# Performance work log

Measured on AMD Instinct MI355X. Metric: run time of the kernel, lower is better.

## Reference

```python
import jax, jax.numpy as jnp
import numpy as np
from jax import lax

FILTER_SIZE = 3
C_IN = 128
C_OUT = 256
PAD = 1
STRIDE = 1


def setup_inputs() -> dict:
    key = jax.random.key(0)
    k1, k2 = jax.random.split(key)
    prev_a = jax.random.normal(k1, (32, 56, 56, C_IN), dtype=jnp.float32)
    # filter_w initialized ~ N(0, 1) as in the original tf.random.normal
    filter_w = jax.random.normal(k2, (FILTER_SIZE, FILTER_SIZE, C_IN, C_OUT), dtype=jnp.float32)
    filter_b = jnp.zeros((1, 1, 1, C_OUT), dtype=jnp.float32)
    return {"prev_a": prev_a, "filter_w": filter_w, "filter_b": filter_b}


def reference(prev_a, filter_w, filter_b):
    # NHWC input, HWIO filter -> NHWC output; same math as the nested-loop conv:
    # z[i,h,w,c] = sum(prev_a_pad[i, h*s:h*s+f, w*s:w*s+f, :] * W[:,:,:,c]) + b[c]
    z = lax.conv_general_dilated(
        prev_a,
        filter_w,
        window_strides=(STRIDE, STRIDE),
        padding=[(PAD, PAD), (PAD, PAD)],
        dimension_numbers=("NHWC", "HWIO", "NHWC"),
    )
    z = z + filter_b  # bias broadcast over (m, H, W)
    return jax.nn.relu(z)
```

## Files before the change

kernel.cpp:

```cpp
#include <hip/hip_runtime.h>
#include <hip/hip_bf16.h>


#define NIMG 32
#define HH 56
#define WW 56
#define PH 58
#define PW 58
#define CIN 128
#define COUT 256
#define KTOT 1152
#define PAD_ELEMS (NIMG * PH * PW * CIN)

#define BM 224
#define BK 64
#define NT (KTOT / BK)
#define NBLK ((NIMG * HH * WW) / BM)

#define AREG_SZ 7168
#define BREG_BASE 28672
#define BREG_SZ 8192

typedef __attribute__((ext_vector_type(8))) short bf16x8;
typedef __attribute__((ext_vector_type(4))) short s16x4;
typedef __attribute__((ext_vector_type(4))) float f32x4;

__device__ __forceinline__ short f2bf(float x) {
    union { __hip_bfloat16 b; short s; } u;
    u.b = __float2bfloat16(x);
    return u.s;
}

typedef const void __attribute__((address_space(1)))* gas1_t;
typedef void __attribute__((address_space(3)))* las3_t;
__device__ __forceinline__ void async16(short* lds_p, const short* g) {
    __builtin_amdgcn_global_load_lds((gas1_t)g, (las3_t)lds_p, 16, 0, 0);
}

__global__ __launch_bounds__(256) void pack_input(const float* __restrict__ in,
                                                  short* __restrict__ pad) {
    const int tid  = blockIdx.x * 256 + threadIdx.x;
    const int flat = tid * 8;
    const int c8   = flat & (CIN - 1);
    const int rest = flat >> 7;
    const int iw   = rest % PW;
    const int r2   = rest / PW;
    const int ih   = r2 % PH;
    const int img  = r2 / PH;
    bf16x8 v = (bf16x8)0;
    if (ih >= 1 && ih <= HH && iw >= 1 && iw <= WW) {
        const float* p = in + (((size_t)(img * HH + ih - 1) * WW + (iw - 1)) * CIN + c8);
        const float4 x0 = *(const float4*)p;
        const float4 x1 = *(const float4*)(p + 4);
        v.s0 = f2bf(x0.x); v.s1 = f2bf(x0.y); v.s2 = f2bf(x0.z); v.s3 = f2bf(x0.w);
        v.s4 = f2bf(x1.x); v.s5 = f2bf(x1.y); v.s6 = f2bf(x1.z); v.s7 = f2bf(x1.w);
    }
    *(bf16x8*)(pad + flat) = v;
}

__global__ __launch_bounds__(256) void pack_wgt(const float* __restrict__ w,
                                                short* __restrict__ wt) {
    __shared__ short tile[32][33];
    const int k0 = blockIdx.x * 32;
    const int n0 = blockIdx.y * 32;
    const int t  = threadIdx.x;
    {
        const int kl  = t >> 3;
        const int nl4 = (t & 7) * 4;
        const float4 x = *(const float4*)(w + (size_t)(k0 + kl) * COUT + n0 + nl4);
        tile[kl][nl4 + 0] = f2bf(x.x);
        tile[kl][nl4 + 1] = f2bf(x.y);
        tile[kl][nl4 + 2] = f2bf(x.z);
        tile[kl][nl4 + 3] = f2bf(x.w);
    }
    __syncthreads();
    {
        const int nl  = t >> 3;
        const int kl4 = (t & 7) * 4;
        s16x4 v;
        v.x = tile[kl4 + 0][nl];
        v.y = tile[kl4 + 1][nl];
        v.z = tile[kl4 + 2][nl];
        v.w = tile[kl4 + 3][nl];
        *(s16x4*)(wt + (size_t)(n0 + nl) * KTOT + k0 + kl4) = v;
    }
}

#define FENCE() asm volatile("" ::: "memory")
#define BARRIER() do { FENCE(); __builtin_amdgcn_s_barrier(); FENCE(); } while (0)
#define VMWAIT(N) asm volatile("s_waitcnt vmcnt(" #N ")" ::: "memory")

__global__ __launch_bounds__(512, 2) void conv_mfma(const short* __restrict__ apad,
                                                    const short* __restrict__ bwt,
                                                    const float* __restrict__ bias,
                                                    float* __restrict__ out) {
    __shared__ short lds[61440];

    const int t  = threadIdx.x;
    const int l  = t & 63;
    const int w  = t >> 6;
    const int wm = w >> 2;
    const int wn = w & 3;
    const int fr = l & 15;
    const int fq = l >> 4;

    const int laneoff = fr * 32 + ((fq ^ ((fr >> 1) & 3))) * 8;
    const int afb = wm * 3584;
    const int bfb = wn * 2048;
    const int kcs = (t & 3) ^ ((t >> 3) & 3);

    const int bid = blockIdx.x;
    const int swz = (bid & 7) * (NBLK / 8) + (bid >> 3);
    const int m0  = swz * BM;

    const int r0 = t >> 2;
    int abase0, abase1;
    {
        int m = m0 + r0;
        int img = m / (HH * WW), rem = m - img * (HH * WW);
        int oh = rem / WW, ow = rem - oh * WW;
        abase0 = ((img * PH + oh) * PW + ow) * CIN;
        if (t < 384) {
            m = m0 + r0 + 128;
            img = m / (HH * WW); rem = m - img * (HH * WW);
            oh = rem / WW; ow = rem - oh * WW;
            abase1 = ((img * PH + oh) * PW + ow) * CIN;
        } else {
            abase1 = abase0;
        }
    }
    const int a2lds = (w < 6) ? (4096 + w * 512) : (w * 512);
    const int bbase0 = r0 * KTOT;
    const int bbase1 = (r0 + 128) * KTOT;

    f32x4 acc[7][4];
#pragma unroll
    for (int i = 0; i < 7; ++i)
#pragma unroll
        for (int j = 0; j < 4; ++j) { f32x4 z = {0.f, 0.f, 0.f, 0.f}; acc[i][j] = z; }

    bf16x8 Aa[7], Ab[7], Ba[4], Bb[4];

#define STAGE(K) do {                                                         \
        const int _tap  = (K) >> 2;                                           \
        const int _fh   = (_tap * 11) >> 5;                  \
        const int _fw   = _tap - 3 * _fh;                                     \
        const int _aoff = (_fh * PW + _fw) * CIN + ((K) & 3) * 32 + kcs * 8;  \
        const int _boff = (K) * 32 + kcs * 8;                                 \
        short* _la = lds + ((K) & 3) * AREG_SZ;                               \
        short* _lb = lds + BREG_BASE + ((K) & 3) * BREG_SZ;                   \
        async16(_la + w * 512, apad + abase0 + _aoff);                        \
        async16(_la + a2lds,   apad + abase1 + _aoff);                        \
        async16(_lb + w * 512,        bwt + bbase0 + _boff);                  \
        async16(_lb + 4096 + w * 512, bwt + bbase1 + _boff);                  \
    } while (0)

#define RD(AF, BF, R) do {                                                    \
        const short* _a = lds + (R) * AREG_SZ;                                \
        const short* _b = lds + BREG_BASE + (R) * BREG_SZ;                    \
        _Pragma("unroll")                                                     \
        for (int _i = 0; _i < 7; ++_i)                                        \
            (AF)[_i] = *(const bf16x8*)(_a + afb + _i * 512 + laneoff);       \
        _Pragma("unroll")                                                     \
        for (int _j = 0; _j < 4; ++_j)                                        \
            (BF)[_j] = *(const bf16x8*)(_b + bfb + _j * 512 + laneoff);       \
    } while (0)

#define MM(AF, BF) do {                                                       \
        __builtin_amdgcn_s_setprio(1);                                        \
        _Pragma("unroll")                                                     \
        for (int _i = 0; _i < 7; ++_i)                                        \
            _Pragma("unroll")                                                 \
            for (int _j = 0; _j < 4; ++_j)                                    \
                acc[_i][_j] = __builtin_amdgcn_mfma_f32_16x16x32_bf16(        \
                    (AF)[_i], (BF)[_j], acc[_i][_j], 0, 0, 0);                \
        __builtin_amdgcn_s_setprio(0);                                        \
    } while (0)

    STAGE(0); STAGE(1); STAGE(2); STAGE(3);
    VMWAIT(8);
    BARRIER();
    RD(Aa, Ba, 0);
    BARRIER();

#pragma unroll 1
    for (int j = 0; j < 8; ++j) {
        const int p0 = j * 4;
        STAGE(p0 + 4); RD(Ab, Bb, 1); MM(Aa, Ba); VMWAIT(8); BARRIER();
        STAGE(p0 + 5); RD(Aa, Ba, 2); MM(Ab, Bb); VMWAIT(8); BARRIER();
        STAGE(p0 + 6); RD(Ab, Bb, 3); MM(Aa, Ba); VMWAIT(8); BARRIER();
        STAGE(p0 + 7); RD(Aa, Ba, 0); MM(Ab, Bb); VMWAIT(8); BARRIER();
    }

    RD(Ab, Bb, 1); MM(Aa, Ba); VMWAIT(4); BARRIER();
    RD(Aa, Ba, 2); MM(Ab, Bb); VMWAIT(0); BARRIER();
    RD(Ab, Bb, 3); MM(Aa, Ba); BARRIER();
    MM(Ab, Bb);

#pragma unroll
    for (int j = 0; j < 4; ++j) {
        const int n  = wn * 64 + j * 16 + fr;
        const float bj = bias[n];
#pragma unroll
        for (int i = 0; i < 7; ++i) {
            const int mr = m0 + wm * 112 + i * 16 + fq * 4;
#pragma unroll
            for (int r = 0; r < 4; ++r) {
                const float v = acc[i][j][r] + bj;
                out[(size_t)(mr + r) * COUT + n] = v > 0.f ? v : 0.f;
            }
        }
    }
#undef STAGE
#undef RD
#undef MM
}

extern "C" void kernel_launch(void* const* d_in, const int* in_sizes, int n_in,
                              void* d_out, int out_size, void* d_ws, size_t ws_size,
                              hipStream_t stream) {
    const float* in   = (const float*)d_in[0];
    const float* wgt  = (const float*)d_in[1];
    const float* bias = (const float*)d_in[2];
    float* out = (float*)d_out;

    short* pad = (short*)d_ws;
    short* wt  = (short*)d_ws + PAD_ELEMS;

    pack_input<<<PAD_ELEMS / 8 / 256, 256, 0, stream>>>(in, pad);
    pack_wgt<<<dim3(KTOT / 32, COUT / 32), 256, 0, stream>>>(wgt, wt);

    conv_mfma<<<NBLK, 512, 0, stream>>>(pad, wt, bias, out);
}
```

Baseline: 202.0 us.

## Halve conv block tile to 112 rows with 256 threads and decoupled A/B staging

Shrinks the output tile per block from 224 to 112 rows and the workgroup from 8 to 4 waves, each wave covering all 112 rows and 64 output channels. A uses a 4-deep LDS ring and B a 3-deep ring, with their prefetch distances staggered, so LDS use drops enough for more blocks to be resident per CU. The intent is better occupancy and latency hiding. The cost is that each block now reloads the full weight tile for half as many rows, doubling B traffic per output.

```diff
diff --git a/kernel.cpp b/kernel.cpp
--- a/kernel.cpp
+++ b/kernel.cpp
@@ -12,13 +12,12 @@
 #define KTOT 1152
 #define PAD_ELEMS (NIMG * PH * PW * CIN)
 
-#define BM 224
-#define BK 64
-#define NT (KTOT / BK)
+#define BM 112
+#define NPHASE 36
 #define NBLK ((NIMG * HH * WW) / BM)
 
-#define AREG_SZ 7168
-#define BREG_BASE 28672
+#define AREG_SZ 3584
+#define BREG_BASE 14336
 #define BREG_SZ 8192
 
 typedef __attribute__((ext_vector_type(8))) short bf16x8;
@@ -90,24 +89,21 @@
 #define BARRIER() do { FENCE(); __builtin_amdgcn_s_barrier(); FENCE(); } while (0)
 #define VMWAIT(N) asm volatile("s_waitcnt vmcnt(" #N ")" ::: "memory")
 
-__global__ __launch_bounds__(512, 2) void conv_mfma(const short* __restrict__ apad,
+__global__ __launch_bounds__(256, 2) void conv_mfma(const short* __restrict__ apad,
                                                     const short* __restrict__ bwt,
                                                     const float* __restrict__ bias,
                                                     float* __restrict__ out) {
-    __shared__ short lds[61440];
+    __shared__ short lds[38912];
 
     const int t  = threadIdx.x;
     const int l  = t & 63;
     const int w  = t >> 6;
-    const int wm = w >> 2;
-    const int wn = w & 3;
     const int fr = l & 15;
     const int fq = l >> 4;
 
     const int laneoff = fr * 32 + ((fq ^ ((fr >> 1) & 3))) * 8;
-    const int afb = wm * 3584;
-    const int bfb = wn * 2048;
-    const int kcs = (t & 3) ^ ((t >> 3) & 3);
+    const int bfb = w * 2048;
+    const int kcs = (l & 3) ^ ((l >> 3) & 3);
 
     const int bid = blockIdx.x;
     const int swz = (bid & 7) * (NBLK / 8) + (bid >> 3);
@@ -120,8 +116,8 @@
         int img = m / (HH * WW), rem = m - img * (HH * WW);
         int oh = rem / WW, ow = rem - oh * WW;
         abase0 = ((img * PH + oh) * PW + ow) * CIN;
-        if (t < 384) {
-            m = m0 + r0 + 128;
+        if (w < 3) {
+            m = m0 + r0 + 64;
             img = m / (HH * WW); rem = m - img * (HH * WW);
             oh = rem / WW; ow = rem - oh * WW;
             abase1 = ((img * PH + oh) * PW + ow) * CIN;
@@ -129,9 +125,8 @@
             abase1 = abase0;
         }
     }
-    const int a2lds = (w < 6) ? (4096 + w * 512) : (w * 512);
-    const int bbase0 = r0 * KTOT;
-    const int bbase1 = (r0 + 128) * KTOT;
+    const int a2lds  = (w < 3) ? (4 + w) * 512 : 3 * 512;
+    const int bbaseB = (w * 64 + (l >> 2)) * KTOT;
 
     f32x4 acc[7][4];
 #pragma unroll
@@ -141,29 +136,36 @@
 
     bf16x8 Aa[7], Ab[7], Ba[4], Bb[4];
 
-#define STAGE(K) do {                                                         \
-        const int _tap  = (K) >> 2;                                           \
-        const int _fh   = (_tap * 11) >> 5;                  \
-        const int _fw   = _tap - 3 * _fh;                                     \
-        const int _aoff = (_fh * PW + _fw) * CIN + ((K) & 3) * 32 + kcs * 8;  \
-        const int _boff = (K) * 32 + kcs * 8;                                 \
-        short* _la = lds + ((K) & 3) * AREG_SZ;                               \
-        short* _lb = lds + BREG_BASE + ((K) & 3) * BREG_SZ;                   \
-        async16(_la + w * 512, apad + abase0 + _aoff);                        \
-        async16(_la + a2lds,   apad + abase1 + _aoff);                        \
-        async16(_lb + w * 512,        bwt + bbase0 + _boff);                  \
-        async16(_lb + 4096 + w * 512, bwt + bbase1 + _boff);                  \
-    } while (0)
-
-#define RD(AF, BF, R) do {                                                    \
-        const short* _a = lds + (R) * AREG_SZ;                                \
-        const short* _b = lds + BREG_BASE + (R) * BREG_SZ;                    \
+#define STAGE_A(K, RG) do {                                                   \
+        const int _kk  = (K) > 35 ? 35 : (K);                                 \
+        const int _tap = _kk >> 2;                                            \
+        const int _fh  = (_tap * 11) >> 5;                   \
+        const int _fw  = _tap - 3 * _fh;                                      \
+        const int _off = (_fh * PW + _fw) * CIN + (_kk & 3) * 32 + kcs * 8;   \
+        short* _l = lds + (RG) * AREG_SZ;                                     \
+        async16(_l + w * 512, apad + abase0 + _off);                          \
+        async16(_l + a2lds,   apad + abase1 + _off);                          \
+    } while (0)
+
+#define STAGE_B(K, RG) do {                                                   \
+        const int _kk  = (K) > 35 ? 35 : (K);                                 \
+        const int _off = _kk * 32 + kcs * 8;                                  \
+        short* _l = lds + BREG_BASE + (RG) * BREG_SZ + w * 2048;              \
+        async16(_l,        bwt + bbaseB + _off);                              \
+        async16(_l + 512,  bwt + bbaseB + 18432 + _off);                      \
+        async16(_l + 1024, bwt + bbaseB + 36864 + _off);                      \
+        async16(_l + 1536, bwt + bbaseB + 55296 + _off);                      \
+    } while (0)
+
+#define RD(AF, BF, AR, BR) do {                                               \
+        const short* _a = lds + (AR) * AREG_SZ;                               \
+        const short* _b = lds + BREG_BASE + (BR) * BREG_SZ + bfb;             \
         _Pragma("unroll")                                                     \
         for (int _i = 0; _i < 7; ++_i)                                        \
-            (AF)[_i] = *(const bf16x8*)(_a + afb + _i * 512 + laneoff);       \
+            (AF)[_i] = *(const bf16x8*)(_a + _i * 512 + laneoff);             \
         _Pragma("unroll")                                                     \
         for (int _j = 0; _j < 4; ++_j)                                        \
-            (BF)[_j] = *(const bf16x8*)(_b + bfb + _j * 512 + laneoff);       \
+            (BF)[_j] = *(const bf16x8*)(_b + _j * 512 + laneoff);             \
     } while (0)
 
 #define MM(AF, BF) do {                                                       \
@@ -177,33 +179,47 @@
         __builtin_amdgcn_s_setprio(0);                                        \
     } while (0)
 
-    STAGE(0); STAGE(1); STAGE(2); STAGE(3);
-    VMWAIT(8);
+#define PHX(KH, ARS, BRS, ARR, BRR, AFc, BFc, AFn, BFn) do {                  \
+        STAGE_A((KH) + 4, ARS);                                               \
+        STAGE_B((KH) + 3, BRS);                                               \
+        RD(AFn, BFn, ARR, BRR);                                               \
+        MM(AFc, BFc);                                                         \
+        VMWAIT(6);                                                            \
+        BARRIER();                                                            \
+    } while (0)
+
+    STAGE_A(0, 0); STAGE_A(1, 1); STAGE_A(2, 2); STAGE_A(3, 3);
+    STAGE_B(0, 0); STAGE_B(1, 1); STAGE_B(2, 2);
+    VMWAIT(4);
     BARRIER();
-    RD(Aa, Ba, 0);
+    RD(Aa, Ba, 0, 0);
     BARRIER();
 
 #pragma unroll 1
-    for (int j = 0; j < 8; ++j) {
-        const int p0 = j * 4;
-        STAGE(p0 + 4); RD(Ab, Bb, 1); MM(Aa, Ba); VMWAIT(8); BARRIER();
-        STAGE(p0 + 5); RD(Aa, Ba, 2); MM(Ab, Bb); VMWAIT(8); BARRIER();
-        STAGE(p0 + 6); RD(Ab, Bb, 3); MM(Aa, Ba); VMWAIT(8); BARRIER();
-        STAGE(p0 + 7); RD(Aa, Ba, 0); MM(Ab, Bb); VMWAIT(8); BARRIER();
-    }
-
-    RD(Ab, Bb, 1); MM(Aa, Ba); VMWAIT(4); BARRIER();
-    RD(Aa, Ba, 2); MM(Ab, Bb); VMWAIT(0); BARRIER();
-    RD(Ab, Bb, 3); MM(Aa, Ba); BARRIER();
-    MM(Ab, Bb);
+    for (int jb = 0; jb < NPHASE; jb += 12) {
+        PHX(jb + 0,  0, 0, 1, 1, Aa, Ba, Ab, Bb);
+        PHX(jb + 1,  1, 1, 2, 2, Ab, Bb, Aa, Ba);
+        PHX(jb + 2,  2, 2, 3, 0, Aa, Ba, Ab, Bb);
+        PHX(jb + 3,  3, 0, 0, 1, Ab, Bb, Aa, Ba);
+        PHX(jb + 4,  0, 1, 1, 2, Aa, Ba, Ab, Bb);
+        PHX(jb + 5,  1, 2, 2, 0, Ab, Bb, Aa, Ba);
+        PHX(jb + 6,  2, 0, 3, 1, Aa, Ba, Ab, Bb);
+        PHX(jb + 7,  3, 1, 0, 2, Ab, Bb, Aa, Ba);
+        PHX(jb + 8,  0, 2, 1, 0, Aa, Ba, Ab, Bb);
+        PHX(jb + 9,  1, 0, 2, 1, Ab, Bb, Aa, Ba);
+        PHX(jb + 10, 2, 1, 3, 2, Aa, Ba, Ab, Bb);
+        PHX(jb + 11, 3, 2, 0, 0, Ab, Bb, Aa, Ba);
+    }
+
+    VMWAIT(0);
 
 #pragma unroll
     for (int j = 0; j < 4; ++j) {
-        const int n  = wn * 64 + j * 16 + fr;
+        const int n  = w * 64 + j * 16 + fr;
         const float bj = bias[n];
 #pragma unroll
         for (int i = 0; i < 7; ++i) {
-            const int mr = m0 + wm * 112 + i * 16 + fq * 4;
+            const int mr = m0 + i * 16 + fq * 4;
 #pragma unroll
             for (int r = 0; r < 4; ++r) {
                 const float v = acc[i][j][r] + bj;
@@ -211,9 +227,11 @@
             }
         }
     }
-#undef STAGE
+#undef STAGE_A
+#undef STAGE_B
 #undef RD
 #undef MM
+#undef PHX
 }
 
 extern "C" void kernel_launch(void* const* d_in, const int* in_sizes, int n_in,
@@ -230,5 +248,5 @@
     pack_input<<<PAD_ELEMS / 8 / 256, 256, 0, stream>>>(in, pad);
     pack_wgt<<<dim3(KTOT / 32, COUT / 32), 256, 0, stream>>>(wgt, wt);
 
-    conv_mfma<<<NBLK, 512, 0, stream>>>(pad, wt, bias, out);
-}
+    conv_mfma<<<NBLK, 256, 0, stream>>>(pad, wt, bias, out);
+}
```

Result: slower. 207.0 us (+2.5%).

## Stage full input window in LDS once and fuse pack kernels

Applied to the files above, without the earlier changes.

The conv kernel now loads each block's whole padded input window (the 224 output pixels plus halo rows, all channels, XOR-swizzled) into LDS once, then reads A fragments for all nine taps straight from that window, so only weight tiles are streamed through a 3-slot ring. The point is to stop re-fetching overlapping input rows from global memory for every tap. The two packing kernels are merged into one launch to cut launch overhead. LDS use per block goes up (about 136 KB), which may limit occupancy to one 512-thread block per CU despite launch_bounds(512,2).

```diff
diff --git a/kernel.cpp b/kernel.cpp
--- a/kernel.cpp
+++ b/kernel.cpp
@@ -13,13 +13,15 @@
 #define PAD_ELEMS (NIMG * PH * PW * CIN)
 
 #define BM 224
-#define BK 64
-#define NT (KTOT / BK)
+#define NPHASE 36
 #define NBLK ((NIMG * HH * WW) / BM)
 
-#define AREG_SZ 7168
-#define BREG_BASE 28672
+#define B_BASE 45056
 #define BREG_SZ 8192
+#define AWIN_CHUNKS 5568
+
+#define NPACK_IN 6728
+#define NPACK_WGT 288
 
 typedef __attribute__((ext_vector_type(8))) short bf16x8;
 typedef __attribute__((ext_vector_type(4))) short s16x4;
@@ -37,52 +39,55 @@
     __builtin_amdgcn_global_load_lds((gas1_t)g, (las3_t)lds_p, 16, 0, 0);
 }
 
-__global__ __launch_bounds__(256) void pack_input(const float* __restrict__ in,
-                                                  short* __restrict__ pad) {
-    const int tid  = blockIdx.x * 256 + threadIdx.x;
-    const int flat = tid * 8;
-    const int c8   = flat & (CIN - 1);
-    const int rest = flat >> 7;
-    const int iw   = rest % PW;
-    const int r2   = rest / PW;
-    const int ih   = r2 % PH;
-    const int img  = r2 / PH;
-    bf16x8 v = (bf16x8)0;
-    if (ih >= 1 && ih <= HH && iw >= 1 && iw <= WW) {
-        const float* p = in + (((size_t)(img * HH + ih - 1) * WW + (iw - 1)) * CIN + c8);
-        const float4 x0 = *(const float4*)p;
-        const float4 x1 = *(const float4*)(p + 4);
-        v.s0 = f2bf(x0.x); v.s1 = f2bf(x0.y); v.s2 = f2bf(x0.z); v.s3 = f2bf(x0.w);
-        v.s4 = f2bf(x1.x); v.s5 = f2bf(x1.y); v.s6 = f2bf(x1.z); v.s7 = f2bf(x1.w);
-    }
-    *(bf16x8*)(pad + flat) = v;
-}
-
-__global__ __launch_bounds__(256) void pack_wgt(const float* __restrict__ w,
-                                                short* __restrict__ wt) {
+__global__ __launch_bounds__(256) void pack_fused(const float* __restrict__ in,
+                                                  short* __restrict__ pad,
+                                                  const float* __restrict__ wsrc,
+                                                  short* __restrict__ wt) {
     __shared__ short tile[32][33];
-    const int k0 = blockIdx.x * 32;
-    const int n0 = blockIdx.y * 32;
+    const int bx = blockIdx.x;
     const int t  = threadIdx.x;
-    {
-        const int kl  = t >> 3;
-        const int nl4 = (t & 7) * 4;
-        const float4 x = *(const float4*)(w + (size_t)(k0 + kl) * COUT + n0 + nl4);
-        tile[kl][nl4 + 0] = f2bf(x.x);
-        tile[kl][nl4 + 1] = f2bf(x.y);
-        tile[kl][nl4 + 2] = f2bf(x.z);
-        tile[kl][nl4 + 3] = f2bf(x.w);
-    }
-    __syncthreads();
-    {
-        const int nl  = t >> 3;
-        const int kl4 = (t & 7) * 4;
-        s16x4 v;
-        v.x = tile[kl4 + 0][nl];
-        v.y = tile[kl4 + 1][nl];
-        v.z = tile[kl4 + 2][nl];
-        v.w = tile[kl4 + 3][nl];
-        *(s16x4*)(wt + (size_t)(n0 + nl) * KTOT + k0 + kl4) = v;
+    if (bx < NPACK_IN) {
+        const int tid  = bx * 256 + t;
+        const int flat = tid * 8;
+        const int c8   = flat & (CIN - 1);
+        const int rest = flat >> 7;
+        const int iw   = rest % PW;
+        const int r2   = rest / PW;
+        const int ih   = r2 % PH;
+        const int img  = r2 / PH;
+        bf16x8 v = (bf16x8)0;
+        if (ih >= 1 && ih <= HH && iw >= 1 && iw <= WW) {
+            const float* p = in + (((size_t)(img * HH + ih - 1) * WW + (iw - 1)) * CIN + c8);
+            const float4 x0 = *(const float4*)p;
+            const float4 x1 = *(const float4*)(p + 4);
+            v.s0 = f2bf(x0.x); v.s1 = f2bf(x0.y); v.s2 = f2bf(x0.z); v.s3 = f2bf(x0.w);
+            v.s4 = f2bf(x1.x); v.s5 = f2bf(x1.y); v.s6 = f2bf(x1.z); v.s7 = f2bf(x1.w);
+        }
+        *(bf16x8*)(pad + flat) = v;
+    } else {
+        const int wb = bx - NPACK_IN;
+        const int k0 = (wb % 36) * 32;
+        const int n0 = (wb / 36) * 32;
+        {
+            const int kl  = t >> 3;
+            const int nl4 = (t & 7) * 4;
+            const float4 x = *(const float4*)(wsrc + (size_t)(k0 + kl) * COUT + n0 + nl4);
+            tile[kl][nl4 + 0] = f2bf(x.x);
+            tile[kl][nl4 + 1] = f2bf(x.y);
+            tile[kl][nl4 + 2] = f2bf(x.z);
+            tile[kl][nl4 + 3] = f2bf(x.w);
+        }
+        __syncthreads();
+        {
+            const int nl  = t >> 3;
+            const int kl4 = (t & 7) * 4;
+            s16x4 v;
+            v.x = tile[kl4 + 0][nl];
+            v.y = tile[kl4 + 1][nl];
+            v.z = tile[kl4 + 2][nl];
+            v.w = tile[kl4 + 3][nl];
+            *(s16x4*)(wt + (size_t)(n0 + nl) * KTOT + k0 + kl4) = v;
+        }
     }
 }
 
@@ -94,7 +99,7 @@
                                                     const short* __restrict__ bwt,
                                                     const float* __restrict__ bias,
                                                     float* __restrict__ out) {
-    __shared__ short lds[61440];
+    __shared__ short lds[69632];
 
     const int t  = threadIdx.x;
     const int l  = t & 63;
@@ -105,7 +110,6 @@
     const int fq = l >> 4;
 
     const int laneoff = fr * 32 + ((fq ^ ((fr >> 1) & 3))) * 8;
-    const int afb = wm * 3584;
     const int bfb = wn * 2048;
     const int kcs = (t & 3) ^ ((t >> 3) & 3);
 
@@ -113,23 +117,21 @@
     const int swz = (bid & 7) * (NBLK / 8) + (bid >> 3);
     const int m0  = swz * BM;
 
+    const int img = m0 / (HH * WW);
+    const int oh0 = (m0 - img * (HH * WW)) / WW;
+    const int gwin = ((img * PH + oh0) * PW) * CIN;
+
+    int abase[7], aow[7];
+#pragma unroll
+    for (int i = 0; i < 7; ++i) {
+        const int mm = (m0 - img * (HH * WW)) + wm * 112 + i * 16 + fr;
+        const int oh = mm / WW;
+        const int ow = mm - oh * WW;
+        abase[i] = ((oh - oh0) * PW + ow) * CIN;
+        aow[i]   = ow;
+    }
+
     const int r0 = t >> 2;
-    int abase0, abase1;
-    {
-        int m = m0 + r0;
-        int img = m / (HH * WW), rem = m - img * (HH * WW);
-        int oh = rem / WW, ow = rem - oh * WW;
-        abase0 = ((img * PH + oh) * PW + ow) * CIN;
-        if (t < 384) {
-            m = m0 + r0 + 128;
-            img = m / (HH * WW); rem = m - img * (HH * WW);
-            oh = rem / WW; ow = rem - oh * WW;
-            abase1 = ((img * PH + oh) * PW + ow) * CIN;
-        } else {
-            abase1 = abase0;
-        }
-    }
-    const int a2lds = (w < 6) ? (4096 + w * 512) : (w * 512);
     const int bbase0 = r0 * KTOT;
     const int bbase1 = (r0 + 128) * KTOT;
 
@@ -141,29 +143,34 @@
 
     bf16x8 Aa[7], Ab[7], Ba[4], Bb[4];
 
-#define STAGE(K) do {                                                         \
-        const int _tap  = (K) >> 2;                                           \
-        const int _fh   = (_tap * 11) >> 5;                  \
-        const int _fw   = _tap - 3 * _fh;                                     \
-        const int _aoff = (_fh * PW + _fw) * CIN + ((K) & 3) * 32 + kcs * 8;  \
-        const int _boff = (K) * 32 + kcs * 8;                                 \
-        short* _la = lds + ((K) & 3) * AREG_SZ;                               \
-        short* _lb = lds + BREG_BASE + ((K) & 3) * BREG_SZ;                   \
-        async16(_la + w * 512, apad + abase0 + _aoff);                        \
-        async16(_la + a2lds,   apad + abase1 + _aoff);                        \
-        async16(_lb + w * 512,        bwt + bbase0 + _boff);                  \
-        async16(_lb + 4096 + w * 512, bwt + bbase1 + _boff);                  \
-    } while (0)
-
-#define RD(AF, BF, R) do {                                                    \
-        const short* _a = lds + (R) * AREG_SZ;                                \
-        const short* _b = lds + BREG_BASE + (R) * BREG_SZ;                    \
+#define STAGE_B(K, RG) do {                                                   \
+        const int _kk  = (K) > 35 ? 35 : (K);                                 \
+        const int _off = _kk * 32 + kcs * 8;                                  \
+        short* _l = lds + B_BASE + (RG) * BREG_SZ;                            \
+        async16(_l + w * 512,        bwt + bbase0 + _off);                    \
+        async16(_l + 4096 + w * 512, bwt + bbase1 + _off);                    \
+    } while (0)
+
+#define RD_A(AF, K1) do {                                                     \
+        const int _kk  = (K1) > 35 ? 35 : (K1);                               \
+        const int _tap = _kk >> 2;                                            \
+        const int _q   = _kk & 3;                                             \
+        const int _fh  = (_tap * 11) >> 5;                                    \
+        const int _fw  = _tap - 3 * _fh;                                      \
+        const int _toff = (_fh * PW + _fw) * CIN;                             \
+        const int _q4 = (_q << 2) | fq;                                       \
         _Pragma("unroll")                                                     \
-        for (int _i = 0; _i < 7; ++_i)                                        \
-            (AF)[_i] = *(const bf16x8*)(_a + afb + _i * 512 + laneoff);       \
+        for (int _i = 0; _i < 7; ++_i) {                                      \
+            const int _phys = _q4 ^ ((aow[_i] + _fw) & 15);                   \
+            (AF)[_i] = *(const bf16x8*)(lds + abase[_i] + _toff + (_phys << 3)); \
+        }                                                                     \
+    } while (0)
+
+#define RD_B(BF, RG) do {                                                     \
+        const short* _b = lds + B_BASE + (RG) * BREG_SZ + bfb;                \
         _Pragma("unroll")                                                     \
         for (int _j = 0; _j < 4; ++_j)                                        \
-            (BF)[_j] = *(const bf16x8*)(_b + bfb + _j * 512 + laneoff);       \
+            (BF)[_j] = *(const bf16x8*)(_b + _j * 512 + laneoff);             \
     } while (0)
 
 #define MM(AF, BF) do {                                                       \
@@ -177,25 +184,41 @@
         __builtin_amdgcn_s_setprio(0);                                        \
     } while (0)
 
-    STAGE(0); STAGE(1); STAGE(2); STAGE(3);
-    VMWAIT(8);
+#define PHZ(C, K, AFc, BFc, AFn, BFn) do {                                    \
+        STAGE_B((K) + 3, (C) % 3);                                            \
+        RD_A(AFn, (K) + 1);                                                   \
+        RD_B(BFn, ((C) + 1) % 3);                                             \
+        MM(AFc, BFc);                                                         \
+        VMWAIT(2);                                                            \
+        BARRIER();                                                            \
+    } while (0)
+
+#pragma unroll
+    for (int j = 0; j < 11; ++j) {
+        const int P  = j * 512 + t;
+        const int Pc = P > (AWIN_CHUNKS - 1) ? (AWIN_CHUNKS - 1) : P;
+        const int cell = Pc >> 4;
+        const int iw   = cell % PW;
+        const int src  = cell * CIN + (((Pc & 15) ^ (iw & 15)) << 3);
+        async16(lds + P * 8, apad + gwin + src);
+    }
+    STAGE_B(0, 0); STAGE_B(1, 1); STAGE_B(2, 2);
+    VMWAIT(2);
     BARRIER();
-    RD(Aa, Ba, 0);
+    RD_A(Aa, 0); RD_B(Ba, 0);
     BARRIER();
 
 #pragma unroll 1
-    for (int j = 0; j < 8; ++j) {
-        const int p0 = j * 4;
-        STAGE(p0 + 4); RD(Ab, Bb, 1); MM(Aa, Ba); VMWAIT(8); BARRIER();
-        STAGE(p0 + 5); RD(Aa, Ba, 2); MM(Ab, Bb); VMWAIT(8); BARRIER();
-        STAGE(p0 + 6); RD(Ab, Bb, 3); MM(Aa, Ba); VMWAIT(8); BARRIER();
-        STAGE(p0 + 7); RD(Aa, Ba, 0); MM(Ab, Bb); VMWAIT(8); BARRIER();
-    }
-
-    RD(Ab, Bb, 1); MM(Aa, Ba); VMWAIT(4); BARRIER();
-    RD(Aa, Ba, 2); MM(Ab, Bb); VMWAIT(0); BARRIER();
-    RD(Ab, Bb, 3); MM(Aa, Ba); BARRIER();
-    MM(Ab, Bb);
+    for (int jb = 0; jb < NPHASE; jb += 6) {
+        PHZ(0, jb + 0, Aa, Ba, Ab, Bb);
+        PHZ(1, jb + 1, Ab, Bb, Aa, Ba);
+        PHZ(2, jb + 2, Aa, Ba, Ab, Bb);
+        PHZ(3, jb + 3, Ab, Bb, Aa, Ba);
+        PHZ(4, jb + 4, Aa, Ba, Ab, Bb);
+        PHZ(5, jb + 5, Ab, Bb, Aa, Ba);
+    }
+
+    VMWAIT(0);
 
 #pragma unroll
     for (int j = 0; j < 4; ++j) {
@@ -211,9 +234,11 @@
             }
         }
     }
-#undef STAGE
-#undef RD
+#undef STAGE_B
+#undef RD_A
+#undef RD_B
 #undef MM
+#undef PHZ
 }
 
 extern "C" void kernel_launch(void* const* d_in, const int* in_sizes, int n_in,
@@ -227,8 +252,7 @@
     short* pad = (short*)d_ws;
     short* wt  = (short*)d_ws + PAD_ELEMS;
 
-    pack_input<<<PAD_ELEMS / 8 / 256, 256, 0, stream>>>(in, pad);
-    pack_wgt<<<dim3(KTOT / 32, COUT / 32), 256, 0, stream>>>(wgt, wt);
+    pack_fused<<<NPACK_IN + NPACK_WGT, 256, 0, stream>>>(in, pad, wgt, wt);
 
     conv_mfma<<<NBLK, 512, 0, stream>>>(pad, wt, bias, out);
 }
```

Measured after the change: 203.3 us. About the same (+0.7%).
